# Performance work log

Measured on AMD Instinct MI355X. Metric: run time of the kernel, lower is better.

Reference implementation:

```python
import jax, jax.numpy as jnp
import numpy as np

DIM = 2048
N_HEADS = 16
HEAD_DIM = DIM // N_HEADS  # 128
HIDDEN = 8192
EPS = 1e-6
NEG = -1e9


def rmsnorm(x, w):
    xf = x.astype(jnp.float32)
    y = xf * jax.lax.rsqrt(jnp.mean(xf * xf, axis=-1, keepdims=True) + EPS)
    return y.astype(x.dtype) * w


def apply_rope(x, cos, sin):
    # x: [B,S,H,Hd]; cos/sin: [S,Hd//2] -> broadcast [1,S,1,Hd//2]
    xf = x.astype(jnp.float32)
    xr = xf[..., 0::2]
    xi = xf[..., 1::2]
    c = cos[None, :, None, :]
    s = sin[None, :, None, :]
    or_ = xr * c - xi * s
    oi_ = xr * s + xi * c
    out = jnp.stack([or_, oi_], axis=-1).reshape(x.shape)
    return out.astype(x.dtype)


def setup_inputs() -> dict:
    key = jax.random.key(0)
    ks = jax.random.split(key, 10)
    B, S = 1, 2048
    x = jax.random.normal(ks[0], (B, S, DIM), dtype=jnp.float32)
    # RoPE frequencies (Llama-style, theta=10000)
    inv_freq = 1.0 / (10000.0 ** (jnp.arange(0, HEAD_DIM, 2, dtype=jnp.float32) / HEAD_DIM))
    angles = jnp.arange(S, dtype=jnp.float32)[:, None] * inv_freq[None, :]  # [S, Hd//2]
    freqs_cos = jnp.cos(angles)
    freqs_sin = jnp.sin(angles)
    # causal additive mask [1,1,S,S]
    mask = jnp.where(jnp.tril(jnp.ones((S, S), dtype=bool)), 0.0, NEG).astype(jnp.float32)[None, None]
    sc = 0.02
    wq = jax.random.normal(ks[1], (DIM, DIM), dtype=jnp.float32) * sc
    wk = jax.random.normal(ks[2], (DIM, DIM), dtype=jnp.float32) * sc
    wv = jax.random.normal(ks[3], (DIM, DIM), dtype=jnp.float32) * sc
    wo = jax.random.normal(ks[4], (DIM, DIM), dtype=jnp.float32) * sc
    w1 = jax.random.normal(ks[5], (DIM, HIDDEN), dtype=jnp.float32) * sc
    w2 = jax.random.normal(ks[6], (HIDDEN, DIM), dtype=jnp.float32) * sc
    w3 = jax.random.normal(ks[7], (DIM, HIDDEN), dtype=jnp.float32) * sc
    attn_norm_w = jnp.ones((DIM,), dtype=jnp.float32)
    ffn_norm_w = jnp.ones((DIM,), dtype=jnp.float32)
    return {"x": x, "freqs_cos": freqs_cos, "freqs_sin": freqs_sin, "mask": mask,
            "wq": wq, "wk": wk, "wv": wv, "wo": wo, "w1": w1, "w2": w2, "w3": w3,
            "attn_norm_w": attn_norm_w, "ffn_norm_w": ffn_norm_w}


def reference(x, freqs_cos, freqs_sin, mask, wq, wk, wv, wo, w1, w2, w3, attn_norm_w, ffn_norm_w):
    B, S, D = x.shape
    # --- attention (pre-norm) ---
    hn = rmsnorm(x, attn_norm_w)
    q = (hn @ wq).reshape(B, S, N_HEADS, HEAD_DIM)
    k = (hn @ wk).reshape(B, S, N_HEADS, HEAD_DIM)
    v = (hn @ wv).reshape(B, S, N_HEADS, HEAD_DIM)
    q = apply_rope(q, freqs_cos, freqs_sin)
    k = apply_rope(k, freqs_cos, freqs_sin)
    scores = jnp.einsum('bqhd,bkhd->bhqk', q, k) / (HEAD_DIM ** 0.5) + mask
    attn = jax.nn.softmax(scores.astype(jnp.float32), axis=-1).astype(q.dtype)
    ctx = jnp.einsum('bhqk,bkhd->bqhd', attn, v).reshape(B, S, D)
    h = x + ctx @ wo
    # --- SwiGLU FFN (pre-norm) ---
    fn = rmsnorm(h, ffn_norm_w)
    ff = (jax.nn.silu(fn @ w1) * (fn @ w3)) @ w2
    return h + ff
```

## Files before the change

### kernel.cpp

```cpp
#include <hip/hip_runtime.h>
#include <hip/hip_bf16.h>

#define DIM 2048
#define HEAD_DIM 128
#define N_HEADS 16
#define SEQ 2048
#define HID 8192
#define SQKV 6144

typedef short bf16x8 __attribute__((ext_vector_type(8)));
typedef float f32x4 __attribute__((ext_vector_type(4)));
using bf16 = __hip_bfloat16;

#define MFMA16(a, b, c) __builtin_amdgcn_mfma_f32_16x16x32_bf16(a, b, c, 0, 0, 0)

__device__ __forceinline__ unsigned short f2bu(float f) {
    union { bf16 b; unsigned short u; } cv;
    cv.b = __float2bfloat16(f);
    return cv.u;
}

__device__ __forceinline__ void gl16(const void* g, void* l) {
    __builtin_amdgcn_global_load_lds(
        (const __attribute__((address_space(1))) unsigned int*)g,
        (__attribute__((address_space(3))) unsigned int*)l, 16, 0, 0);
}

__global__ __launch_bounds__(256) void rmsnorm_bf16_k(
    const float* __restrict__ x, const float* __restrict__ w, bf16* __restrict__ y)
{
    const int row = blockIdx.x;
    const int tid = threadIdx.x;
    const float* xr = x + (size_t)row * DIM;
    float4 v0 = ((const float4*)xr)[tid];
    float4 v1 = ((const float4*)xr)[tid + 256];
    float ss = v0.x*v0.x + v0.y*v0.y + v0.z*v0.z + v0.w*v0.w
             + v1.x*v1.x + v1.y*v1.y + v1.z*v1.z + v1.w*v1.w;
    for (int o = 32; o > 0; o >>= 1) ss += __shfl_down(ss, o);
    __shared__ float red[4];
    if ((tid & 63) == 0) red[tid >> 6] = ss;
    __syncthreads();
    float tot = red[0] + red[1] + red[2] + red[3];
    float r = rsqrtf(tot * (1.0f / DIM) + 1e-6f);
    float4 w0 = ((const float4*)w)[tid];
    float4 w1 = ((const float4*)w)[tid + 256];
    ushort4 o0, o1;
    o0.x = f2bu(v0.x * r * w0.x); o0.y = f2bu(v0.y * r * w0.y);
    o0.z = f2bu(v0.z * r * w0.z); o0.w = f2bu(v0.w * r * w0.w);
    o1.x = f2bu(v1.x * r * w1.x); o1.y = f2bu(v1.y * r * w1.y);
    o1.z = f2bu(v1.z * r * w1.z); o1.w = f2bu(v1.w * r * w1.w);
    ushort4* yr = (ushort4*)(y + (size_t)row * DIM);
    yr[tid] = o0;
    yr[tid + 256] = o1;
}

__global__ __launch_bounds__(256) void rmsnorm4_k(
    const float* __restrict__ part, const float* __restrict__ x,
    const float* __restrict__ w, float* __restrict__ hout, bf16* __restrict__ y)
{
    const int row = blockIdx.x;
    const int tid = threadIdx.x;
    const size_t base = (size_t)row * DIM;
    const size_t SP = (size_t)SEQ * DIM;
    float4 r0, r1;
    float ss = 0.0f;
    {
        float4 a  = ((const float4*)(x + base))[tid];
        float4 p0 = ((const float4*)(part + base))[tid];
        float4 p1 = ((const float4*)(part + SP + base))[tid];
        float4 p2 = ((const float4*)(part + 2 * SP + base))[tid];
        float4 p3 = ((const float4*)(part + 3 * SP + base))[tid];
        r0.x = a.x + ((p0.x + p1.x) + (p2.x + p3.x));
        r0.y = a.y + ((p0.y + p1.y) + (p2.y + p3.y));
        r0.z = a.z + ((p0.z + p1.z) + (p2.z + p3.z));
        r0.w = a.w + ((p0.w + p1.w) + (p2.w + p3.w));
        ((float4*)(hout + base))[tid] = r0;
        ss += r0.x*r0.x + r0.y*r0.y + r0.z*r0.z + r0.w*r0.w;
    }
    {
        const int t2 = tid + 256;
        float4 a  = ((const float4*)(x + base))[t2];
        float4 p0 = ((const float4*)(part + base))[t2];
        float4 p1 = ((const float4*)(part + SP + base))[t2];
        float4 p2 = ((const float4*)(part + 2 * SP + base))[t2];
        float4 p3 = ((const float4*)(part + 3 * SP + base))[t2];
        r1.x = a.x + ((p0.x + p1.x) + (p2.x + p3.x));
        r1.y = a.y + ((p0.y + p1.y) + (p2.y + p3.y));
        r1.z = a.z + ((p0.z + p1.z) + (p2.z + p3.z));
        r1.w = a.w + ((p0.w + p1.w) + (p2.w + p3.w));
        ((float4*)(hout + base))[t2] = r1;
        ss += r1.x*r1.x + r1.y*r1.y + r1.z*r1.z + r1.w*r1.w;
    }
    for (int o = 32; o > 0; o >>= 1) ss += __shfl_down(ss, o);
    __shared__ float red[4];
    if ((tid & 63) == 0) red[tid >> 6] = ss;
    __syncthreads();
    float tot = red[0] + red[1] + red[2] + red[3];
    float r = rsqrtf(tot * (1.0f / DIM) + 1e-6f);
    float4 w0 = ((const float4*)w)[tid];
    float4 w1 = ((const float4*)w)[tid + 256];
    ushort4 o0, o1;
    o0.x = f2bu(r0.x * r * w0.x); o0.y = f2bu(r0.y * r * w0.y);
    o0.z = f2bu(r0.z * r * w0.z); o0.w = f2bu(r0.w * r * w0.w);
    o1.x = f2bu(r1.x * r * w1.x); o1.y = f2bu(r1.y * r * w1.y);
    o1.z = f2bu(r1.z * r * w1.z); o1.w = f2bu(r1.w * r * w1.w);
    ushort4* yr = (ushort4*)(y + base);
    yr[tid] = o0;
    yr[tid + 256] = o1;
}

__global__ __launch_bounds__(256) void reduce4_k(
    const float* __restrict__ part, const float* __restrict__ h, float* __restrict__ out)
{
    const size_t i = (size_t)blockIdx.x * 256 + threadIdx.x;
    const size_t SP4 = (size_t)SEQ * DIM / 4;
    float4 a  = ((const float4*)h)[i];
    float4 p0 = ((const float4*)part)[i];
    float4 p1 = ((const float4*)part)[i + SP4];
    float4 p2 = ((const float4*)part)[i + 2 * SP4];
    float4 p3 = ((const float4*)part)[i + 3 * SP4];
    float4 r;
    r.x = a.x + ((p0.x + p1.x) + (p2.x + p3.x));
    r.y = a.y + ((p0.y + p1.y) + (p2.y + p3.y));
    r.z = a.z + ((p0.z + p1.z) + (p2.z + p3.z));
    r.w = a.w + ((p0.w + p1.w) + (p2.w + p3.w));
    ((float4*)out)[i] = r;
}

__global__ __launch_bounds__(256) void convT_f32_bf16_k(
    const float* __restrict__ in, bf16* __restrict__ out, int R, int C)
{
    __shared__ float t[32][33];
    const int tx = threadIdx.x, ty = threadIdx.y;
    const int x0 = blockIdx.x * 32, y0 = blockIdx.y * 32;
#pragma unroll
    for (int i = 0; i < 4; ++i)
        t[ty + i * 8][tx] = in[(size_t)(y0 + ty + i * 8) * C + x0 + tx];
    __syncthreads();
#pragma unroll
    for (int i = 0; i < 4; ++i)
        out[(size_t)(x0 + ty + i * 8) * R + y0 + tx] = __float2bfloat16(t[tx][ty + i * 8]);
}

__global__ __launch_bounds__(256) void convT3_f32_bf16_k(
    const float* __restrict__ wq, const float* __restrict__ wk,
    const float* __restrict__ wv, bf16* __restrict__ out)
{
    const int z = blockIdx.z;
    const float* in = z == 0 ? wq : (z == 1 ? wk : wv);
    bf16* o = out + (size_t)z * DIM * DIM;
    __shared__ float t[32][33];
    const int tx = threadIdx.x, ty = threadIdx.y;
    const int x0 = blockIdx.x * 32, y0 = blockIdx.y * 32;
#pragma unroll
    for (int i = 0; i < 4; ++i)
        t[ty + i * 8][tx] = in[(size_t)(y0 + ty + i * 8) * DIM + x0 + tx];
    __syncthreads();
#pragma unroll
    for (int i = 0; i < 4; ++i)
        o[(size_t)(x0 + ty + i * 8) * DIM + y0 + tx] = __float2bfloat16(t[tx][ty + i * 8]);
}

__global__ __launch_bounds__(256) void transpose_bf16_k(
    const bf16* __restrict__ in, int istride, bf16* __restrict__ out)
{
    __shared__ unsigned short t[32][33];
    const int tx = threadIdx.x, ty = threadIdx.y;
    const int x = blockIdx.x * 32 + tx;
    const int y0 = blockIdx.y * 32;
    const unsigned short* inu = (const unsigned short*)in;
    unsigned short* outu = (unsigned short*)out;
#pragma unroll
    for (int i = 0; i < 4; ++i)
        t[ty + i * 8][tx] = inu[(size_t)(y0 + ty + i * 8) * istride + x];
    __syncthreads();
    const int x2 = blockIdx.y * 32 + tx;
    const int y2 = blockIdx.x * 32;
#pragma unroll
    for (int i = 0; i < 4; ++i)
        outu[(size_t)(y2 + ty + i * 8) * SEQ + x2] = t[tx][ty + i * 8];
}

__global__ __launch_bounds__(256) void rope_qk_k(
    bf16* __restrict__ q, bf16* __restrict__ k,
    const float* __restrict__ cosb, const float* __restrict__ sinb)
{
    const int gid = blockIdx.x * 256 + threadIdx.x;
    const int s = gid >> 10;
    const int p = gid & 1023;
    const int h = p >> 6, j = p & 63;
    const size_t off = (size_t)s * SQKV + h * HEAD_DIM + 2 * j;
    const float c = cosb[s * 64 + j], sn = sinb[s * 64 + j];
    float xr = __bfloat162float(q[off]), xi = __bfloat162float(q[off + 1]);
    q[off]     = __float2bfloat16(xr * c - xi * sn);
    q[off + 1] = __float2bfloat16(xr * sn + xi * c);
    xr = __bfloat162float(k[off]); xi = __bfloat162float(k[off + 1]);
    k[off]     = __float2bfloat16(xr * c - xi * sn);
    k[off + 1] = __float2bfloat16(xr * sn + xi * c);
}

template <int EP>
__global__ __launch_bounds__(512, 1) void gemm256_k(
    const bf16* __restrict__ A, const bf16* __restrict__ Bt, const bf16* __restrict__ Bt2,
    bf16* __restrict__ Cb, float* __restrict__ Pf,
    int M, int N, int K, int gx, int ntile, int Ks)
{
    extern __shared__ char smem[];
    const int t512 = threadIdx.x;
    const int w = t512 >> 6, lane = t512 & 63;
    const int lr = lane & 15, lg = lane >> 4;
    const int wm = w >> 2, wn = w & 3;
    const int bofs = (wn & 1) * 64;
    const int swz = (lr & 7) << 4;

    const int nwg = gridDim.x;
    const int q8 = nwg >> 3, r8 = nwg & 7;
    const int xcd = blockIdx.x & 7, seqq = blockIdx.x >> 3;
    const int wgid = (xcd < r8 ? xcd * (q8 + 1) : r8 * (q8 + 1) + (xcd - r8) * q8) + seqq;
    const int split = wgid / ntile;
    const int tile = wgid % ntile;
    const int grp = tile / (4 * gx), rem = tile % (4 * gx);
    const int m0 = (grp * 4 + (rem & 3)) * 256, n0 = (rem >> 2) * 256;
    const int kb0 = split * Ks;
    const int niter = Ks >> 7;

    const bf16* aS[2][2]; const bf16* bS[2][2];
    int sOff[2];
#pragma unroll
    for (int c = 0; c < 2; ++c) {
        const int s = (c * 512 + t512) * 16;
        const int pp = s ^ (((s >> 7) & 7) << 4);
        const int row = pp >> 7, colE = (pp & 127) >> 1;
        sOff[c] = s;
#pragma unroll
        for (int hs = 0; hs < 2; ++hs) {
            aS[hs][c] = A + (size_t)(m0 + hs * 128 + row) * K + kb0 + colE;
            const int rg = n0 + hs * 128 + row;
            if (EP == 4) {
                const int g = rg >> 4;
                const bf16* src = (g & 1) ? Bt2 : Bt;
                const int j = ((g >> 1) << 4) + (rg & 15);
                bS[hs][c] = src + (size_t)j * K + kb0 + colE;
            } else {
                bS[hs][c] = Bt + (size_t)rg * K + kb0 + colE;
            }
        }
    }
    auto stA = [&](int buf, int kt, int hs) {
        char* base = smem + (buf * 2 + hs) * 16384;
        gl16(aS[hs][0] + (kt << 6), base + sOff[0]);
        gl16(aS[hs][1] + (kt << 6), base + sOff[1]);
    };
    auto stB = [&](int buf, int kt, int hs) {
        char* base = smem + 65536 + (buf * 2 + hs) * 16384;
        gl16(bS[hs][0] + (kt << 6), base + sOff[0]);
        gl16(bS[hs][1] + (kt << 6), base + sOff[1]);
    };

    const char* A0m = smem + (0 * 2 + wm) * 16384;
    const char* A1m = smem + (1 * 2 + wm) * 16384;
    const char* B0m = smem + 65536 + (0 * 2 + (wn >> 1)) * 16384;
    const char* B1m = smem + 65536 + (1 * 2 + (wn >> 1)) * 16384;

    f32x4 acc[8][4] = {};
    bf16x8 bfr[4][2];
    bf16x8 x0, x1, x2, x3;

#define SBAR __builtin_amdgcn_s_barrier()
#define LGKM0 do { asm volatile("s_waitcnt lgkmcnt(0)" ::: "memory"); \
                   __builtin_amdgcn_sched_barrier(0); } while (0)
#define LGKM8 do { asm volatile("s_waitcnt lgkmcnt(8)" ::: "memory"); \
                   __builtin_amdgcn_sched_barrier(0); } while (0)
#define WVM(n) do { asm volatile("s_waitcnt vmcnt(" #n ")" ::: "memory"); \
                    __builtin_amdgcn_sched_barrier(0); } while (0)
#define LDA4(base, mf0) do { \
    x0 = *(const bf16x8*)((base) + (((mf0) * 16 + lr) * 128) + ((lg * 16) ^ swz)); \
    x1 = *(const bf16x8*)((base) + (((mf0) * 16 + lr) * 128) + ((64 + lg * 16) ^ swz)); \
    x2 = *(const bf16x8*)((base) + ((((mf0) + 1) * 16 + lr) * 128) + ((lg * 16) ^ swz)); \
    x3 = *(const bf16x8*)((base) + ((((mf0) + 1) * 16 + lr) * 128) + ((64 + lg * 16) ^ swz)); \
    } while (0)
#define LDB8(base) do { \
    _Pragma("unroll") \
    for (int nf = 0; nf < 4; ++nf) { \
        bfr[nf][0] = *(const bf16x8*)((base) + ((bofs + nf * 16 + lr) * 128) + ((lg * 16) ^ swz)); \
        bfr[nf][1] = *(const bf16x8*)((base) + ((bofs + nf * 16 + lr) * 128) + ((64 + lg * 16) ^ swz)); \
    } } while (0)
#define MFMA_PH(mf0) do { \
    __builtin_amdgcn_s_setprio(1); \
    _Pragma("unroll") \
    for (int nf = 0; nf < 4; ++nf) { \
        acc[(mf0)][nf]     = MFMA16(x0, bfr[nf][0], acc[(mf0)][nf]); \
        acc[(mf0)][nf]     = MFMA16(x1, bfr[nf][1], acc[(mf0)][nf]); \
        acc[(mf0) + 1][nf] = MFMA16(x2, bfr[nf][0], acc[(mf0) + 1][nf]); \
        acc[(mf0) + 1][nf] = MFMA16(x3, bfr[nf][1], acc[(mf0) + 1][nf]); \
    } \
    __builtin_amdgcn_s_setprio(0); } while (0)

    stB(0, 0, 0); stB(0, 0, 1); stA(0, 0, 0); stA(0, 0, 1);
    stB(1, 1, 0); stB(1, 1, 1);
    WVM(4);
    SBAR;

    for (int t = 0; t < niter; ++t) {
        const bool pf = (t + 1 < niter);
        const int k1 = 2 * t + 1, k2 = 2 * t + 2, k3 = 2 * t + 3;

        LDB8(B0m);
        LDA4(A0m, 0);
        stA(1, k1, 0);
        LGKM8;
        SBAR; LGKM0; MFMA_PH(0); SBAR;
        LDA4(A0m, 2);
        stA(1, k1, 1);
        SBAR; LGKM0; MFMA_PH(2); SBAR;
        LDA4(A0m, 4);
        if (pf) stB(0, k2, 0);
        SBAR; LGKM0; MFMA_PH(4); SBAR;
        if (pf) { WVM(2); } else { WVM(0); }
        LDA4(A0m, 6);
        if (pf) stB(0, k2, 1);
        SBAR; LGKM0; MFMA_PH(6); SBAR;
        LDB8(B1m);
        LDA4(A1m, 0);
        if (pf) stA(0, k2, 0);
        LGKM8;
        SBAR; LGKM0; MFMA_PH(0); SBAR;
        LDA4(A1m, 2);
        if (pf) stA(0, k2, 1);
        SBAR; LGKM0; MFMA_PH(2); SBAR;
        LDA4(A1m, 4);
        if (pf) stB(1, k3, 0);
        SBAR; LGKM0; MFMA_PH(4); SBAR;
        if (pf) WVM(2);
        LDA4(A1m, 6);
        if (pf) stB(1, k3, 1);
        SBAR; LGKM0; MFMA_PH(6); SBAR;
    }
#undef SBAR
#undef LGKM0
#undef LGKM8
#undef WVM
#undef LDA4
#undef LDB8
#undef MFMA_PH

    if (EP == 4) {
        const int jb = (n0 >> 1) + wn * 32;
        const int NH = N >> 1;
#pragma unroll
        for (int mf = 0; mf < 8; ++mf)
#pragma unroll
            for (int pp = 0; pp < 4; pp += 2) {
                const int row = m0 + wm * 128 + mf * 16 + lg * 4;
                const int j = jb + (pp >> 1) * 16 + lr;
#pragma unroll
                for (int r = 0; r < 4; ++r) {
                    const float a = acc[mf][pp][r];
                    const float b = acc[mf][pp + 1][r];
                    const float s = a / (1.0f + __expf(-a));
                    Cb[(size_t)(row + r) * NH + j] = __float2bfloat16(s * b);
                }
            }
    } else {
        float* pf_base = Pf + (size_t)split * M * N;
#pragma unroll
        for (int mf = 0; mf < 8; ++mf)
#pragma unroll
            for (int nf = 0; nf < 4; ++nf) {
                const int row = m0 + wm * 128 + mf * 16 + lg * 4;
                const int col = n0 + wn * 64 + nf * 16 + lr;
#pragma unroll
                for (int r = 0; r < 4; ++r) {
                    const size_t idx = (size_t)(row + r) * N + col;
                    const float v = acc[mf][nf][r];
                    if (EP == 0) Cb[idx] = __float2bfloat16(v);
                    else         pf_base[idx] = v;
                }
            }
    }
}

__global__ __launch_bounds__(512) void attn_fwd_k(
    const bf16* __restrict__ qkv, const bf16* __restrict__ vT, bf16* __restrict__ ctx)
{
    const int tid = threadIdx.x;
    const int w8 = tid >> 6, lane = tid & 63;
    const int lr = lane & 15, lg = lane >> 4;
    const int w = w8 & 3, tsel = w8 >> 2;
    const int h = blockIdx.y;
    const int bx = blockIdx.x;
    const int qidx = tsel ? (31 - bx) : bx;
    const int q0b = qidx * 64;
    const int myNt = qidx + 1;
    const int nt = 32 - bx;

    __shared__ __align__(16) unsigned short Kt[2][64 * 128];
    __shared__ __align__(16) unsigned short Vt[128 * 64];
    __shared__ __align__(16) unsigned short Pp[8][16 * 64];

    const char* kbase = (const char*)(qkv + DIM + h * HEAD_DIM);
    const char* vbase = (const char*)(vT + (size_t)h * HEAD_DIM * SEQ);

    const int krow_c = tid >> 4;
    const int kcolB  = (tid & 15) * 16;
    const int vrow_c = tid >> 3;
    const int vcolB  = (tid & 7) * 16;

    auto stageK = [&](int buf, int kb) {
#pragma unroll
        for (int c = 0; c < 2; ++c) {
            const int r = c * 32 + krow_c;
            gl16(kbase + (size_t)(kb + r) * (SQKV * 2) + (kcolB ^ ((r & 7) << 4)),
                 &Kt[buf][c * 4096 + tid * 8]);
        }
    };
    auto stageV = [&](int kb) {
#pragma unroll
        for (int c = 0; c < 2; ++c) {
            const int r = c * 64 + vrow_c;
            gl16(vbase + (size_t)r * (SEQ * 2) + kb * 2 + (vcolB ^ ((r & 7) << 4)),
                 &Vt[c * 4096 + tid * 8]);
        }
    };

    bf16x8 qf[4];
    const bf16* qrow = qkv + (size_t)(q0b + w * 16 + lr) * SQKV + h * HEAD_DIM;
#pragma unroll
    for (int dt = 0; dt < 4; ++dt)
        qf[dt] = *(const bf16x8*)(qrow + dt * 32 + lg * 8);

    f32x4 o[8] = {};
    float m[4], l[4];
#pragma unroll
    for (int j = 0; j < 4; ++j) { m[j] = -3e38f; l[j] = 0.0f; }
    const float scale = 0.08838834764831845f;

    stageK(0, 0);
    asm volatile("s_waitcnt vmcnt(0)" ::: "memory");
    __builtin_amdgcn_sched_barrier(0);
    __builtin_amdgcn_s_barrier();

    int cur = 0;
    for (int t = 0; t < nt; ++t) {
        const int kb = t * 64;
        const bool pf = (t + 1 < nt);
        stageV(kb);
        if (pf) stageK(cur ^ 1, kb + 64);
        const bool act = (t < myNt);

        if (act) {
            f32x4 s[4] = {};
            __builtin_amdgcn_s_setprio(1);
#pragma unroll
            for (int ss = 0; ss < 4; ++ss) {
                const int r = ss * 16 + lr;
                const int sw = (r & 7) << 3;
#pragma unroll
                for (int dt = 0; dt < 4; ++dt) {
                    bf16x8 kf = *(const bf16x8*)&Kt[cur][r * 128 + ((dt * 32 + lg * 8) ^ sw)];
                    s[ss] = MFMA16(qf[dt], kf, s[ss]);
                }
            }
            __builtin_amdgcn_s_setprio(0);

            float al[4];
#pragma unroll
            for (int j = 0; j < 4; ++j) {
                const int qi = q0b + w * 16 + lg * 4 + j;
                const int prow = lg * 4 + j;
                const int psw = (prow & 7) << 3;
                float a[4];
#pragma unroll
                for (int ss = 0; ss < 4; ++ss)
                    a[ss] = s[ss][j] * scale + ((kb + ss * 16 + lr) > qi ? -1e9f : 0.0f);
                float mx = fmaxf(fmaxf(a[0], a[1]), fmaxf(a[2], a[3]));
                mx = fmaxf(mx, __shfl_xor(mx, 1));
                mx = fmaxf(mx, __shfl_xor(mx, 2));
                mx = fmaxf(mx, __shfl_xor(mx, 4));
                mx = fmaxf(mx, __shfl_xor(mx, 8));
                const float mn = fmaxf(m[j], mx);
                const float asc = __expf(m[j] - mn);
                float e0 = __expf(a[0] - mn), e1 = __expf(a[1] - mn);
                float e2 = __expf(a[2] - mn), e3 = __expf(a[3] - mn);
                float rs = (e0 + e1) + (e2 + e3);
                rs += __shfl_xor(rs, 1); rs += __shfl_xor(rs, 2);
                rs += __shfl_xor(rs, 4); rs += __shfl_xor(rs, 8);
                l[j] = l[j] * asc + rs;
                m[j] = mn;
                al[j] = asc;
                Pp[w8][prow * 64 + ((lr)      ^ psw)] = f2bu(e0);
                Pp[w8][prow * 64 + ((16 + lr) ^ psw)] = f2bu(e1);
                Pp[w8][prow * 64 + ((32 + lr) ^ psw)] = f2bu(e2);
                Pp[w8][prow * 64 + ((48 + lr) ^ psw)] = f2bu(e3);
            }
#pragma unroll
            for (int d2 = 0; d2 < 8; ++d2)
#pragma unroll
                for (int j = 0; j < 4; ++j) o[d2][j] *= al[j];
        }

        if (pf) { asm volatile("s_waitcnt vmcnt(2)" ::: "memory"); }
        else    { asm volatile("s_waitcnt vmcnt(0)" ::: "memory"); }
        __builtin_amdgcn_sched_barrier(0);
        __builtin_amdgcn_s_barrier();

        if (act) {
            asm volatile("s_waitcnt lgkmcnt(0)" ::: "memory");
            __builtin_amdgcn_sched_barrier(0);
            const int asw = (lr & 7) << 3;
            bf16x8 pa0 = *(const bf16x8*)&Pp[w8][lr * 64 + ((lg * 8)      ^ asw)];
            bf16x8 pa1 = *(const bf16x8*)&Pp[w8][lr * 64 + ((32 + lg * 8) ^ asw)];

            __builtin_amdgcn_s_setprio(1);
#pragma unroll
            for (int d2 = 0; d2 < 8; ++d2) {
                const int rv = d2 * 16 + lr;
                const int vsw = (rv & 7) << 3;
                bf16x8 vf0 = *(const bf16x8*)&Vt[rv * 64 + ((lg * 8)      ^ vsw)];
                bf16x8 vf1 = *(const bf16x8*)&Vt[rv * 64 + ((32 + lg * 8) ^ vsw)];
                o[d2] = MFMA16(pa0, vf0, o[d2]);
                o[d2] = MFMA16(pa1, vf1, o[d2]);
            }
            __builtin_amdgcn_s_setprio(0);
        }

        __builtin_amdgcn_s_barrier();
        cur ^= 1;
    }

#pragma unroll
    for (int j = 0; j < 4; ++j) {
        const float inv = 1.0f / l[j];
        bf16* dst = ctx + (size_t)(q0b + w * 16 + lg * 4 + j) * DIM + h * HEAD_DIM + lr;
#pragma unroll
        for (int d2 = 0; d2 < 8; ++d2)
            dst[d2 * 16] = __float2bfloat16(o[d2][j] * inv);
    }
}

extern "C" void kernel_launch(void* const* d_in, const int* in_sizes, int n_in,
                              void* d_out, int out_size, void* d_ws, size_t ws_size,
                              hipStream_t stream)
{
    const float* x   = (const float*)d_in[0];
    const float* fc  = (const float*)d_in[1];
    const float* fs  = (const float*)d_in[2];
    const float* wq  = (const float*)d_in[4];
    const float* wk  = (const float*)d_in[5];
    const float* wv  = (const float*)d_in[6];
    const float* wo  = (const float*)d_in[7];
    const float* w1  = (const float*)d_in[8];
    const float* w2  = (const float*)d_in[9];
    const float* w3  = (const float*)d_in[10];
    const float* anw = (const float*)d_in[11];
    const float* fnw = (const float*)d_in[12];
    float* out = (float*)d_out;

    char* p = (char*)d_ws;
    auto alloc = [&](size_t n) { char* r = p; p += (n + 255) & ~(size_t)255; return r; };
    bf16* wT  = (bf16*)alloc((size_t)HID * DIM * 2);
    bf16* hn  = (bf16*)alloc((size_t)SEQ * DIM * 2);
    bf16* qkv = (bf16*)alloc((size_t)SEQ * SQKV * 2);
    bf16* vt  = (bf16*)alloc((size_t)SEQ * DIM * 2);
    bf16* ctx = (bf16*)alloc((size_t)SEQ * DIM * 2);
    bf16* fn  = (bf16*)alloc((size_t)SEQ * DIM * 2);
    float* h  = (float*)alloc((size_t)SEQ * DIM * 4);
    bf16* g   = (bf16*)alloc((size_t)SEQ * HID * 2);
    float* sk = (float*)alloc((size_t)4 * SEQ * DIM * 4);
    bf16* w3T = hn;

    const dim3 tb32(32, 8);
    const int LDS256 = 131072;
    (void)hipFuncSetAttribute((const void*)gemm256_k<0>,
        hipFuncAttributeMaxDynamicSharedMemorySize, LDS256);
    (void)hipFuncSetAttribute((const void*)gemm256_k<3>,
        hipFuncAttributeMaxDynamicSharedMemorySize, LDS256);
    (void)hipFuncSetAttribute((const void*)gemm256_k<4>,
        hipFuncAttributeMaxDynamicSharedMemorySize, LDS256);

    rmsnorm_bf16_k<<<SEQ, 256, 0, stream>>>(x, anw, hn);

    convT3_f32_bf16_k<<<dim3(DIM / 32, DIM / 32, 3), tb32, 0, stream>>>(wq, wk, wv, wT);
    gemm256_k<0><<<(SEQ / 256) * (SQKV / 256), 512, LDS256, stream>>>(
        hn, wT, nullptr, qkv, nullptr, SEQ, SQKV, DIM, SQKV / 256, (SEQ / 256) * (SQKV / 256), DIM);

    rope_qk_k<<<(SEQ * 1024) / 256, 256, 0, stream>>>(qkv, qkv + DIM, fc, fs);
    transpose_bf16_k<<<dim3(DIM / 32, SEQ / 32), tb32, 0, stream>>>(qkv + 2 * DIM, SQKV, vt);

    attn_fwd_k<<<dim3(16, N_HEADS), 512, 0, stream>>>(qkv, vt, ctx);

    convT_f32_bf16_k<<<dim3(DIM / 32, DIM / 32), tb32, 0, stream>>>(wo, wT, DIM, DIM);
    gemm256_k<3><<<(SEQ / 256) * (DIM / 256) * 4, 512, LDS256, stream>>>(
        ctx, wT, nullptr, nullptr, sk, SEQ, DIM, DIM, DIM / 256, (SEQ / 256) * (DIM / 256), 512);
    rmsnorm4_k<<<SEQ, 256, 0, stream>>>(sk, x, fnw, h, fn);

    convT_f32_bf16_k<<<dim3(HID / 32, DIM / 32), tb32, 0, stream>>>(w1, wT, DIM, HID);
    convT_f32_bf16_k<<<dim3(HID / 32, DIM / 32), tb32, 0, stream>>>(w3, w3T, DIM, HID);
    gemm256_k<4><<<(SEQ / 256) * ((2 * HID) / 256), 512, LDS256, stream>>>(
        fn, wT, w3T, g, nullptr, SEQ, 2 * HID, DIM, (2 * HID) / 256,
        (SEQ / 256) * ((2 * HID) / 256), DIM);

    convT_f32_bf16_k<<<dim3(DIM / 32, HID / 32), tb32, 0, stream>>>(w2, wT, HID, DIM);
    gemm256_k<3><<<(SEQ / 256) * (DIM / 256) * 4, 512, LDS256, stream>>>(
        g, wT, nullptr, nullptr, sk, SEQ, DIM, HID, DIM / 256, (SEQ / 256) * (DIM / 256), 2048);
    reduce4_k<<<(SEQ * DIM / 4) / 256, 256, 0, stream>>>(sk, h, out);
}
```

Before: 477.0 us.

## Store split-K partials in bf16 and widen weight-transpose tiles to 64x64

Split-K GEMM partial sums are now written as bf16 instead of fp32, halving the partial-buffer traffic in the GEMM epilogue and in the two reduction kernels. The weight convert-transpose kernels use 64x64 tiles with float4 loads and 16-byte bf16 stores, and the w1/w3 transposes are merged into one launch. The risk is lower precision in the partial sums before the fp32 reduction.

```diff
diff --git a/kernel.cpp b/kernel.cpp
--- a/kernel.cpp
+++ b/kernel.cpp
@@ -18,6 +18,11 @@
     union { bf16 b; unsigned short u; } cv;
     cv.b = __float2bfloat16(f);
     return cv.u;
+}
+__device__ __forceinline__ float bu2f(unsigned short u) {
+    union { unsigned short u; bf16 b; } cv;
+    cv.u = u;
+    return __bfloat162float(cv.b);
 }
 
 __device__ __forceinline__ void gl16(const void* g, void* l) {
@@ -55,117 +60,126 @@
 }
 
 __global__ __launch_bounds__(256) void rmsnorm4_k(
-    const float* __restrict__ part, const float* __restrict__ x,
+    const bf16* __restrict__ part, const float* __restrict__ x,
     const float* __restrict__ w, float* __restrict__ hout, bf16* __restrict__ y)
 {
     const int row = blockIdx.x;
     const int tid = threadIdx.x;
-    const size_t base = (size_t)row * DIM;
+    const size_t base = (size_t)row * DIM + tid * 8;
     const size_t SP = (size_t)SEQ * DIM;
-    float4 r0, r1;
+    float4 a0 = *(const float4*)(x + base);
+    float4 a1 = *(const float4*)(x + base + 4);
+    bf16x8 p0 = *(const bf16x8*)(part + base);
+    bf16x8 p1 = *(const bf16x8*)(part + SP + base);
+    bf16x8 p2 = *(const bf16x8*)(part + 2 * SP + base);
+    bf16x8 p3 = *(const bf16x8*)(part + 3 * SP + base);
+    float r8[8];
     float ss = 0.0f;
-    {
-        float4 a  = ((const float4*)(x + base))[tid];
-        float4 p0 = ((const float4*)(part + base))[tid];
-        float4 p1 = ((const float4*)(part + SP + base))[tid];
-        float4 p2 = ((const float4*)(part + 2 * SP + base))[tid];
-        float4 p3 = ((const float4*)(part + 3 * SP + base))[tid];
-        r0.x = a.x + ((p0.x + p1.x) + (p2.x + p3.x));
-        r0.y = a.y + ((p0.y + p1.y) + (p2.y + p3.y));
-        r0.z = a.z + ((p0.z + p1.z) + (p2.z + p3.z));
-        r0.w = a.w + ((p0.w + p1.w) + (p2.w + p3.w));
-        ((float4*)(hout + base))[tid] = r0;
-        ss += r0.x*r0.x + r0.y*r0.y + r0.z*r0.z + r0.w*r0.w;
-    }
-    {
-        const int t2 = tid + 256;
-        float4 a  = ((const float4*)(x + base))[t2];
-        float4 p0 = ((const float4*)(part + base))[t2];
-        float4 p1 = ((const float4*)(part + SP + base))[t2];
-        float4 p2 = ((const float4*)(part + 2 * SP + base))[t2];
-        float4 p3 = ((const float4*)(part + 3 * SP + base))[t2];
-        r1.x = a.x + ((p0.x + p1.x) + (p2.x + p3.x));
-        r1.y = a.y + ((p0.y + p1.y) + (p2.y + p3.y));
-        r1.z = a.z + ((p0.z + p1.z) + (p2.z + p3.z));
-        r1.w = a.w + ((p0.w + p1.w) + (p2.w + p3.w));
-        ((float4*)(hout + base))[t2] = r1;
-        ss += r1.x*r1.x + r1.y*r1.y + r1.z*r1.z + r1.w*r1.w;
-    }
+#pragma unroll
+    for (int e = 0; e < 8; ++e) {
+        const float xa = e < 4 ? (&a0.x)[e] : (&a1.x)[e - 4];
+        const float v = xa + ((bu2f((unsigned short)p0[e]) + bu2f((unsigned short)p1[e]))
+                            + (bu2f((unsigned short)p2[e]) + bu2f((unsigned short)p3[e])));
+        r8[e] = v;
+        ss += v * v;
+    }
+    *(float4*)(hout + base)     = make_float4(r8[0], r8[1], r8[2], r8[3]);
+    *(float4*)(hout + base + 4) = make_float4(r8[4], r8[5], r8[6], r8[7]);
     for (int o = 32; o > 0; o >>= 1) ss += __shfl_down(ss, o);
     __shared__ float red[4];
     if ((tid & 63) == 0) red[tid >> 6] = ss;
     __syncthreads();
     float tot = red[0] + red[1] + red[2] + red[3];
     float r = rsqrtf(tot * (1.0f / DIM) + 1e-6f);
-    float4 w0 = ((const float4*)w)[tid];
-    float4 w1 = ((const float4*)w)[tid + 256];
-    ushort4 o0, o1;
-    o0.x = f2bu(r0.x * r * w0.x); o0.y = f2bu(r0.y * r * w0.y);
-    o0.z = f2bu(r0.z * r * w0.z); o0.w = f2bu(r0.w * r * w0.w);
-    o1.x = f2bu(r1.x * r * w1.x); o1.y = f2bu(r1.y * r * w1.y);
-    o1.z = f2bu(r1.z * r * w1.z); o1.w = f2bu(r1.w * r * w1.w);
-    ushort4* yr = (ushort4*)(y + base);
-    yr[tid] = o0;
-    yr[tid + 256] = o1;
+    float4 w0 = *(const float4*)(w + tid * 8);
+    float4 w1 = *(const float4*)(w + tid * 8 + 4);
+    bf16x8 o8;
+#pragma unroll
+    for (int e = 0; e < 8; ++e) {
+        const float ww = e < 4 ? (&w0.x)[e] : (&w1.x)[e - 4];
+        o8[e] = (short)f2bu(r8[e] * r * ww);
+    }
+    *(bf16x8*)((unsigned short*)y + base) = o8;
 }
 
 __global__ __launch_bounds__(256) void reduce4_k(
-    const float* __restrict__ part, const float* __restrict__ h, float* __restrict__ out)
-{
-    const size_t i = (size_t)blockIdx.x * 256 + threadIdx.x;
-    const size_t SP4 = (size_t)SEQ * DIM / 4;
-    float4 a  = ((const float4*)h)[i];
-    float4 p0 = ((const float4*)part)[i];
-    float4 p1 = ((const float4*)part)[i + SP4];
-    float4 p2 = ((const float4*)part)[i + 2 * SP4];
-    float4 p3 = ((const float4*)part)[i + 3 * SP4];
-    float4 r;
-    r.x = a.x + ((p0.x + p1.x) + (p2.x + p3.x));
-    r.y = a.y + ((p0.y + p1.y) + (p2.y + p3.y));
-    r.z = a.z + ((p0.z + p1.z) + (p2.z + p3.z));
-    r.w = a.w + ((p0.w + p1.w) + (p2.w + p3.w));
-    ((float4*)out)[i] = r;
-}
-
-__global__ __launch_bounds__(256) void convT_f32_bf16_k(
+    const bf16* __restrict__ part, const float* __restrict__ h, float* __restrict__ out)
+{
+    const size_t i = ((size_t)blockIdx.x * 256 + threadIdx.x) * 8;
+    const size_t SP = (size_t)SEQ * DIM;
+    float4 a0 = *(const float4*)(h + i);
+    float4 a1 = *(const float4*)(h + i + 4);
+    bf16x8 p0 = *(const bf16x8*)(part + i);
+    bf16x8 p1 = *(const bf16x8*)(part + SP + i);
+    bf16x8 p2 = *(const bf16x8*)(part + 2 * SP + i);
+    bf16x8 p3 = *(const bf16x8*)(part + 3 * SP + i);
+    float r8[8];
+#pragma unroll
+    for (int e = 0; e < 8; ++e) {
+        const float xa = e < 4 ? (&a0.x)[e] : (&a1.x)[e - 4];
+        r8[e] = xa + ((bu2f((unsigned short)p0[e]) + bu2f((unsigned short)p1[e]))
+                    + (bu2f((unsigned short)p2[e]) + bu2f((unsigned short)p3[e])));
+    }
+    *(float4*)(out + i)     = make_float4(r8[0], r8[1], r8[2], r8[3]);
+    *(float4*)(out + i + 4) = make_float4(r8[4], r8[5], r8[6], r8[7]);
+}
+
+__device__ __forceinline__ void convT64_body(
+    const float* __restrict__ in, bf16* __restrict__ out, int R, int C,
+    int bx, int by)
+{
+    __shared__ unsigned short t[64][72];
+    const int tid = threadIdx.x;
+    const int x0 = bx * 64;
+    const int y0 = by * 64;
+    const int tx = tid & 15, ty = tid >> 4;
+#pragma unroll
+    for (int i = 0; i < 4; ++i) {
+        const int row = ty + i * 16;
+        float4 v = *(const float4*)(in + (size_t)(y0 + row) * C + x0 + tx * 4);
+        t[tx * 4 + 0][row] = f2bu(v.x);
+        t[tx * 4 + 1][row] = f2bu(v.y);
+        t[tx * 4 + 2][row] = f2bu(v.z);
+        t[tx * 4 + 3][row] = f2bu(v.w);
+    }
+    __syncthreads();
+    const int rx = tid & 7, cy = tid >> 3;
+#pragma unroll
+    for (int i = 0; i < 2; ++i) {
+        const int c = cy + i * 32;
+        bf16x8 v = *(const bf16x8*)&t[c][rx * 8];
+        *(bf16x8*)(out + (size_t)(x0 + c) * R + y0 + rx * 8) = v;
+    }
+}
+
+__global__ __launch_bounds__(256) void convT64_k(
     const float* __restrict__ in, bf16* __restrict__ out, int R, int C)
 {
-    __shared__ float t[32][33];
-    const int tx = threadIdx.x, ty = threadIdx.y;
-    const int x0 = blockIdx.x * 32, y0 = blockIdx.y * 32;
-#pragma unroll
-    for (int i = 0; i < 4; ++i)
-        t[ty + i * 8][tx] = in[(size_t)(y0 + ty + i * 8) * C + x0 + tx];
-    __syncthreads();
-#pragma unroll
-    for (int i = 0; i < 4; ++i)
-        out[(size_t)(x0 + ty + i * 8) * R + y0 + tx] = __float2bfloat16(t[tx][ty + i * 8]);
-}
-
-__global__ __launch_bounds__(256) void convT3_f32_bf16_k(
+    convT64_body(in, out, R, C, blockIdx.x, blockIdx.y);
+}
+
+__global__ __launch_bounds__(256) void convT64q_k(
     const float* __restrict__ wq, const float* __restrict__ wk,
     const float* __restrict__ wv, bf16* __restrict__ out)
 {
     const int z = blockIdx.z;
     const float* in = z == 0 ? wq : (z == 1 ? wk : wv);
-    bf16* o = out + (size_t)z * DIM * DIM;
-    __shared__ float t[32][33];
-    const int tx = threadIdx.x, ty = threadIdx.y;
-    const int x0 = blockIdx.x * 32, y0 = blockIdx.y * 32;
-#pragma unroll
-    for (int i = 0; i < 4; ++i)
-        t[ty + i * 8][tx] = in[(size_t)(y0 + ty + i * 8) * DIM + x0 + tx];
-    __syncthreads();
-#pragma unroll
-    for (int i = 0; i < 4; ++i)
-        o[(size_t)(x0 + ty + i * 8) * DIM + y0 + tx] = __float2bfloat16(t[tx][ty + i * 8]);
+    convT64_body(in, out + (size_t)z * DIM * DIM, DIM, DIM, blockIdx.x, blockIdx.y);
+}
+
+__global__ __launch_bounds__(256) void convT64f_k(
+    const float* __restrict__ w1, const float* __restrict__ w3,
+    bf16* __restrict__ o1, bf16* __restrict__ o3)
+{
+    const int z = blockIdx.z;
+    convT64_body(z ? w3 : w1, z ? o3 : o1, DIM, HID, blockIdx.x, blockIdx.y);
 }
 
 __global__ __launch_bounds__(256) void transpose_bf16_k(
     const bf16* __restrict__ in, int istride, bf16* __restrict__ out)
 {
     __shared__ unsigned short t[32][33];
-    const int tx = threadIdx.x, ty = threadIdx.y;
+    const int tx = threadIdx.x & 31, ty = threadIdx.x >> 5;
     const int x = blockIdx.x * 32 + tx;
     const int y0 = blockIdx.y * 32;
     const unsigned short* inu = (const unsigned short*)in;
@@ -202,7 +216,7 @@
 template <int EP>
 __global__ __launch_bounds__(512, 1) void gemm256_k(
     const bf16* __restrict__ A, const bf16* __restrict__ Bt, const bf16* __restrict__ Bt2,
-    bf16* __restrict__ Cb, float* __restrict__ Pf,
+    bf16* __restrict__ Cb,
     int M, int N, int K, int gx, int ntile, int Ks)
 {
     extern __shared__ char smem[];
@@ -362,7 +376,7 @@
                 }
             }
     } else {
-        float* pf_base = Pf + (size_t)split * M * N;
+        bf16* cb = (EP == 3) ? Cb + (size_t)split * M * N : Cb;
 #pragma unroll
         for (int mf = 0; mf < 8; ++mf)
 #pragma unroll
@@ -370,12 +384,8 @@
                 const int row = m0 + wm * 128 + mf * 16 + lg * 4;
                 const int col = n0 + wn * 64 + nf * 16 + lr;
 #pragma unroll
-                for (int r = 0; r < 4; ++r) {
-                    const size_t idx = (size_t)(row + r) * N + col;
-                    const float v = acc[mf][nf][r];
-                    if (EP == 0) Cb[idx] = __float2bfloat16(v);
-                    else         pf_base[idx] = v;
-                }
+                for (int r = 0; r < 4; ++r)
+                    cb[(size_t)(row + r) * N + col] = __float2bfloat16(acc[mf][nf][r]);
             }
     }
 }
@@ -566,10 +576,9 @@
     bf16* fn  = (bf16*)alloc((size_t)SEQ * DIM * 2);
     float* h  = (float*)alloc((size_t)SEQ * DIM * 4);
     bf16* g   = (bf16*)alloc((size_t)SEQ * HID * 2);
-    float* sk = (float*)alloc((size_t)4 * SEQ * DIM * 4);
+    bf16* sk  = (bf16*)alloc((size_t)4 * SEQ * DIM * 2);
     bf16* w3T = hn;
 
-    const dim3 tb32(32, 8);
     const int LDS256 = 131072;
     (void)hipFuncSetAttribute((const void*)gemm256_k<0>,
         hipFuncAttributeMaxDynamicSharedMemorySize, LDS256);
@@ -580,28 +589,27 @@
 
     rmsnorm_bf16_k<<<SEQ, 256, 0, stream>>>(x, anw, hn);
 
-    convT3_f32_bf16_k<<<dim3(DIM / 32, DIM / 32, 3), tb32, 0, stream>>>(wq, wk, wv, wT);
+    convT64q_k<<<dim3(DIM / 64, DIM / 64, 3), 256, 0, stream>>>(wq, wk, wv, wT);
     gemm256_k<0><<<(SEQ / 256) * (SQKV / 256), 512, LDS256, stream>>>(
-        hn, wT, nullptr, qkv, nullptr, SEQ, SQKV, DIM, SQKV / 256, (SEQ / 256) * (SQKV / 256), DIM);
+        hn, wT, nullptr, qkv, SEQ, SQKV, DIM, SQKV / 256, (SEQ / 256) * (SQKV / 256), DIM);
 
     rope_qk_k<<<(SEQ * 1024) / 256, 256, 0, stream>>>(qkv, qkv + DIM, fc, fs);
-    transpose_bf16_k<<<dim3(DIM / 32, SEQ / 32), tb32, 0, stream>>>(qkv + 2 * DIM, SQKV, vt);
+    transpose_bf16_k<<<dim3(DIM / 32, SEQ / 32), 256, 0, stream>>>(qkv + 2 * DIM, SQKV, vt);
 
     attn_fwd_k<<<dim3(16, N_HEADS), 512, 0, stream>>>(qkv, vt, ctx);
 
-    convT_f32_bf16_k<<<dim3(DIM / 32, DIM / 32), tb32, 0, stream>>>(wo, wT, DIM, DIM);
+    convT64_k<<<dim3(DIM / 64, DIM / 64), 256, 0, stream>>>(wo, wT, DIM, DIM);
     gemm256_k<3><<<(SEQ / 256) * (DIM / 256) * 4, 512, LDS256, stream>>>(
-        ctx, wT, nullptr, nullptr, sk, SEQ, DIM, DIM, DIM / 256, (SEQ / 256) * (DIM / 256), 512);
+        ctx, wT, nullptr, sk, SEQ, DIM, DIM, DIM / 256, (SEQ / 256) * (DIM / 256), 512);
     rmsnorm4_k<<<SEQ, 256, 0, stream>>>(sk, x, fnw, h, fn);
 
-    convT_f32_bf16_k<<<dim3(HID / 32, DIM / 32), tb32, 0, stream>>>(w1, wT, DIM, HID);
-    convT_f32_bf16_k<<<dim3(HID / 32, DIM / 32), tb32, 0, stream>>>(w3, w3T, DIM, HID);
+    convT64f_k<<<dim3(HID / 64, DIM / 64, 2), 256, 0, stream>>>(w1, w3, wT, w3T);
     gemm256_k<4><<<(SEQ / 256) * ((2 * HID) / 256), 512, LDS256, stream>>>(
-        fn, wT, w3T, g, nullptr, SEQ, 2 * HID, DIM, (2 * HID) / 256,
+        fn, wT, w3T, g, SEQ, 2 * HID, DIM, (2 * HID) / 256,
         (SEQ / 256) * ((2 * HID) / 256), DIM);
 
-    convT_f32_bf16_k<<<dim3(DIM / 32, HID / 32), tb32, 0, stream>>>(w2, wT, HID, DIM);
+    convT64_k<<<dim3(DIM / 64, HID / 64), 256, 0, stream>>>(w2, wT, HID, DIM);
     gemm256_k<3><<<(SEQ / 256) * (DIM / 256) * 4, 512, LDS256, stream>>>(
-        g, wT, nullptr, nullptr, sk, SEQ, DIM, HID, DIM / 256, (SEQ / 256) * (DIM / 256), 2048);
-    reduce4_k<<<(SEQ * DIM / 4) / 256, 256, 0, stream>>>(sk, h, out);
-}
+        g, wT, nullptr, sk, SEQ, DIM, HID, DIM / 256, (SEQ / 256) * (DIM / 256), 2048);
+    reduce4_k<<<(SEQ * DIM / 8) / 256, 256, 0, stream>>>(sk, h, out);
+}
```

Result: faster. 448.3 us (-6.0%).
